# Optimization experiments

Measured on AMD Instinct MI355X. Metric: run time of the kernel, lower is better.

The kernel has to match this reference:

```python
import jax, jax.numpy as jnp
import numpy as np

B, S, D = 2, 2048, 1024
N, M, HD = 16, 4, 64          # query heads, kv heads, head dim
G = N // M                    # GQA group size
V = 32000
GIN = 12                      # gate input dim
ROPE_THETA = 1024.0
ROT = int(HD * 0.5)           # partial rotary dim = 32
EPS = 1e-6
STD = 0.006


def setup_inputs() -> dict:
    key = jax.random.key(0)
    ks = jax.random.split(key, 10)
    tn = lambda k, shape: (STD * jax.random.truncated_normal(k, -3, 3, shape)).astype(jnp.float32)
    return {
        "x": jax.random.normal(ks[0], (B, S, D), jnp.float32),
        "token_ids": jax.random.randint(ks[1], (B, S), 0, V),
        "mask": jnp.tril(jnp.ones((S, S), dtype=bool)),  # causal
        "w_q": tn(ks[2], (D, N * HD)),
        "w_k": tn(ks[3], (D, M * HD)),
        "w_v": tn(ks[4], (D, M * HD)),
        "w_o": tn(ks[5], (N * HD, D)),  # zeros at init; random for a meaningful baseline
        "ve_embed": tn(ks[6], (V, M * HD)),
        "value_lambda": jnp.full((), 0.5, jnp.float32),
        "ve_lambda": jnp.full((), 0.5, jnp.float32),
        "ve_gate": tn(ks[7], (GIN, M)),
        "attn_gate": tn(ks[8], (GIN, N)),
    }


def _qk_norm(t):
    var = jnp.mean(jnp.square(t.astype(jnp.float32)), axis=-1, keepdims=True)
    return (t * jax.lax.rsqrt(var + EPS)).astype(t.dtype)


def _rope(t):
    # partial rotary: rotate first ROT dims only
    half = ROT // 2
    inv_freq = 1.0 / ROPE_THETA ** (jnp.arange(half, dtype=jnp.float32) / half)
    ang = jnp.arange(S, dtype=jnp.float32)[:, None] * inv_freq[None, :]
    cos = jnp.cos(ang)[None, :, None, :]  # [1,S,1,half]
    sin = jnp.sin(ang)[None, :, None, :]
    rot, pas = t[..., :ROT], t[..., ROT:]
    x1, x2 = jnp.split(rot, 2, axis=-1)
    return jnp.concatenate([x1 * cos - x2 * sin, x2 * cos + x1 * sin, pas], axis=-1)


def reference(x, token_ids, mask, w_q, w_k, w_v, w_o, ve_embed,
              value_lambda, ve_lambda, ve_gate, attn_gate):
    q = (x @ w_q).reshape(B, S, N, HD)
    k = (x @ w_k).reshape(B, S, M, HD)
    v = (x @ w_v).reshape(B, S, M, HD)
    q = _rope(_qk_norm(q))
    k = _rope(_qk_norm(k))

    # value-embedding lambda mixing with sigmoid gate
    ve = ve_embed[token_ids].reshape(B, S, M, HD)
    ve_g = 2.0 * jax.nn.sigmoid(x[..., :GIN] @ ve_gate)       # [B,S,M]
    v = value_lambda * v + ve_lambda * ve_g[..., None] * ve

    # GQA causal attention (group q heads over kv heads, no kv repeat)
    qg = q.reshape(B, S, M, G, HD)
    scale = 1.0 / np.sqrt(HD).astype(np.float32)
    scores = jnp.einsum('bqmgd,bkmd->bmgqk', qg, k) * scale   # [B,M,G,S,S]
    scores = jnp.where(mask[None, None, None], scores, jnp.float32(-1e30))
    p = jax.nn.softmax(scores, axis=-1)
    attn = jnp.einsum('bmgqk,bkmd->bqmgd', p, v).reshape(B, S, N, HD)

    # output sigmoid gate then out-projection
    a_g = 2.0 * jax.nn.sigmoid(x[..., :GIN] @ attn_gate)      # [B,S,N]
    attn = a_g[..., None] * attn
    return attn.reshape(B, S, N * HD) @ w_o
```

## Files before the change

### kernel.cpp

```cpp
#include <hip/hip_runtime.h>
#include <math.h>

#define S_LEN 2048
#define NHEADS 16
#define KVH 4

typedef __attribute__((ext_vector_type(8))) _Float16 half8;
typedef __attribute__((ext_vector_type(4))) _Float16 half4;
typedef __attribute__((ext_vector_type(2))) __fp16 fp16x2;
typedef __attribute__((ext_vector_type(4))) float f32x4;

__device__ inline void gld16(const void* g, void* l) {
  __builtin_amdgcn_global_load_lds(
      (const __attribute__((address_space(1))) unsigned int*)g,
      (__attribute__((address_space(3))) unsigned int*)l, 16, 0, 0);
}

__global__ __launch_bounds__(256) void setup_fused(
    const float* __restrict__ wq, const float* __restrict__ wk,
    const float* __restrict__ wv, const float* __restrict__ wo,
    const float* __restrict__ x, const float* __restrict__ attn_gate,
    _Float16* __restrict__ wqkvT, _Float16* __restrict__ woT,
    float2* __restrict__ costab, float* __restrict__ ag,
    _Float16* __restrict__ xh)
{
  const int t = threadIdx.x;
  int L = blockIdx.x;

  if (L >= 1024) {
    const size_t i = ((size_t)(L - 1024) * 256 + t) * 16;
    #pragma unroll
    for (int c = 0; c < 2; c++) {
      float4 f0 = *(const float4*)(x + i + c * 8);
      float4 f1 = *(const float4*)(x + i + c * 8 + 4);
      half8 h;
      h[0] = (_Float16)f0.x; h[1] = (_Float16)f0.y; h[2] = (_Float16)f0.z; h[3] = (_Float16)f0.w;
      h[4] = (_Float16)f1.x; h[5] = (_Float16)f1.y; h[6] = (_Float16)f1.z; h[7] = (_Float16)f1.w;
      *(half8*)(xh + i + c * 8) = h;
    }
    return;
  }
  if (L >= 768) {
    const int row = (L - 768) * 16 + (t >> 4);
    const int n = t & 15;
    float z = 0.f;
    #pragma unroll
    for (int i = 0; i < 12; ++i) z += x[(size_t)row * 1024 + i] * attn_gate[i * NHEADS + n];
    ag[(size_t)row * NHEADS + n] = 2.f / (1.f + __expf(-z));
    return;
  }
  if (L >= 640) {
    const int gi = (L - 640) * 256 + t;
    const int s = gi >> 4, i = gi & 15;
    const float ang = (float)s * exp2f(-0.625f * (float)i);
    float c, sn;
    sincosf(ang, &sn, &c);
    costab[gi] = make_float2(c, sn);
    return;
  }

  const float* in; _Float16* out; int C, ct, rt;
  if (L < 256)      { in = wq; out = wqkvT;                       C = 1024; ct = (L & 15) * 64; rt = (L >> 4) * 64; }
  else if (L < 320) { L -= 256; in = wk; out = wqkvT + (size_t)1024 * 1024; C = 256; ct = (L & 3) * 64; rt = (L >> 2) * 64; }
  else if (L < 384) { L -= 320; in = wv; out = wqkvT + (size_t)1280 * 1024; C = 256; ct = (L & 3) * 64; rt = (L >> 2) * 64; }
  else              { L -= 384; in = wo; out = woT;               C = 1024; ct = (L & 15) * 64; rt = (L >> 4) * 64; }

  __shared__ float Ls[64][65];
  {
    const int r = t >> 2, cs = (t & 3) << 4;
    const float* src = in + (size_t)(rt + r) * C + ct + cs;
    #pragma unroll
    for (int j = 0; j < 16; j += 4) {
      float4 v = *(const float4*)(src + j);
      Ls[r][cs + j] = v.x; Ls[r][cs + j + 1] = v.y;
      Ls[r][cs + j + 2] = v.z; Ls[r][cs + j + 3] = v.w;
    }
  }
  __syncthreads();
  {
    const int c = t >> 2, rs = (t & 3) << 4;
    half8 h0, h1;
    #pragma unroll
    for (int j = 0; j < 8; j++) h0[j] = (_Float16)Ls[rs + j][c];
    #pragma unroll
    for (int j = 0; j < 8; j++) h1[j] = (_Float16)Ls[rs + 8 + j][c];
    _Float16* dst = out + (size_t)(ct + c) * 1024 + rt + rs;
    *(half8*)dst = h0;
    *(half8*)(dst + 8) = h1;
  }
}

template<typename OUT_T, bool EPI>
__global__ __launch_bounds__(256) void gemm_k(
    const _Float16* __restrict__ A, const _Float16* __restrict__ BT,
    OUT_T* __restrict__ C, int M, int N, int K, int lda,
    const float2* __restrict__ costab)
{
  __shared__ _Float16 lds[24576];
  const int t = threadIdx.x;
  const int w = t >> 6, l = t & 63;
  const int lg = l >> 4, ll = l & 15;
  const int bm = blockIdx.y * 64, bn = blockIdx.x * 128;
  const int wr = (w >> 1) * 32, wc = (w & 1) * 64;
  const int srow = l >> 3, sslot = l & 7;

  f32x4 acc[2][4] = {};

  auto stage = [&](int k0, int buf) {
    char* Ab = (char*)lds + buf * 8192;
    char* Bb = (char*)lds + 16384 + buf * 16384;
    #pragma unroll
    for (int i = 0; i < 2; i++) {
      const int row = w * 16 + i * 8 + srow;
      gld16(A + (size_t)(bm + row) * lda + k0 + ((sslot ^ (row & 7)) << 3),
            Ab + w * 2048 + i * 1024);
    }
    #pragma unroll
    for (int i = 0; i < 4; i++) {
      const int row = w * 32 + i * 8 + srow;
      gld16(BT + (size_t)(bn + row) * K + k0 + ((sslot ^ (row & 7)) << 3),
            Bb + w * 4096 + i * 1024);
    }
  };

  stage(0, 0);
  __syncthreads();

  int buf = 0;
  for (int k0 = 0; k0 < K; k0 += 64) {
    if (k0 + 64 < K) stage(k0 + 64, buf ^ 1);

    const char* Ab = (const char*)lds + buf * 8192;
    const char* Bb = (const char*)lds + 16384 + buf * 16384;
    half8 af[2][2], bfr[2][4];
    #pragma unroll
    for (int mt = 0; mt < 2; mt++) {
      const int row = wr + mt * 16 + ll;
      #pragma unroll
      for (int s = 0; s < 2; s++)
        af[mt][s] = *(const half8*)(Ab + row * 128 + (((4 * s + lg) ^ (row & 7)) << 4));
    }
    #pragma unroll
    for (int nt = 0; nt < 4; nt++) {
      const int row = wc + nt * 16 + ll;
      #pragma unroll
      for (int s = 0; s < 2; s++)
        bfr[s][nt] = *(const half8*)(Bb + row * 128 + (((4 * s + lg) ^ (row & 7)) << 4));
    }
    __builtin_amdgcn_s_setprio(1);
    #pragma unroll
    for (int s = 0; s < 2; s++)
      #pragma unroll
      for (int mt = 0; mt < 2; mt++)
        #pragma unroll
        for (int nt = 0; nt < 4; nt++)
          acc[mt][nt] = __builtin_amdgcn_mfma_f32_16x16x32_f16(af[mt][s], bfr[s][nt], acc[mt][nt], 0, 0, 0);
    __builtin_amdgcn_s_setprio(0);

    __syncthreads();
    buf ^= 1;
  }

  if constexpr (EPI) {
    const int col0 = bn + wc;
    const int head = col0 >> 6;
    const bool isv = head >= 20;
    const float qs = (head < 16) ? 0.18033688f : 1.0f;
    #pragma unroll
    for (int mt = 0; mt < 2; mt++) {
      if (isv) {
        #pragma unroll
        for (int r = 0; r < 4; r++) {
          const size_t row = (size_t)bm + wr + mt * 16 + lg * 4 + r;
          #pragma unroll
          for (int nt = 0; nt < 4; nt++)
            C[row * N + col0 + nt * 16 + ll] = (OUT_T)acc[mt][nt][r];
        }
      } else {
        float ss[4];
        #pragma unroll
        for (int r = 0; r < 4; r++)
          ss[r] = acc[mt][0][r] * acc[mt][0][r] + acc[mt][1][r] * acc[mt][1][r]
                + acc[mt][2][r] * acc[mt][2][r] + acc[mt][3][r] * acc[mt][3][r];
        #pragma unroll
        for (int mi = 0; mi < 4; mi++) {
          const int msk = 1 << mi;
          #pragma unroll
          for (int r = 0; r < 4; r++) ss[r] += __shfl_xor(ss[r], msk);
        }
        #pragma unroll
        for (int r = 0; r < 4; r++) {
          const size_t row = (size_t)bm + wr + mt * 16 + lg * 4 + r;
          const float inv = rsqrtf(ss[r] * (1.0f / 64.0f) + 1e-6f) * qs;
          const float2 cs2 = costab[(row & (S_LEN - 1)) * 16 + ll];
          const float a0 = acc[mt][0][r] * inv, a1 = acc[mt][1][r] * inv;
          C[row * N + col0 +      ll] = (OUT_T)(a0 * cs2.x - a1 * cs2.y);
          C[row * N + col0 + 16 + ll] = (OUT_T)(a1 * cs2.x + a0 * cs2.y);
          C[row * N + col0 + 32 + ll] = (OUT_T)(acc[mt][2][r] * inv);
          C[row * N + col0 + 48 + ll] = (OUT_T)(acc[mt][3][r] * inv);
        }
      }
    }
  } else {
    #pragma unroll
    for (int mt = 0; mt < 2; mt++) {
      #pragma unroll
      for (int r = 0; r < 4; r++) {
        const size_t row = (size_t)bm + wr + mt * 16 + lg * 4 + r;
        #pragma unroll
        for (int nt = 0; nt < 4; nt++) {
          const int col = bn + wc + nt * 16 + ll;
          if constexpr (sizeof(OUT_T) == 2) C[row * N + col] = (OUT_T)(_Float16)acc[mt][nt][r];
          else                              C[row * N + col] = acc[mt][nt][r];
        }
      }
    }
  }
}

__global__ __launch_bounds__(256) void vtrans_mix(
    const _Float16* __restrict__ qkv, const float* __restrict__ x,
    const int* __restrict__ token_ids, const float* __restrict__ ve_embed,
    const float* __restrict__ ve_gate, const float* __restrict__ vlam,
    const float* __restrict__ velam, _Float16* __restrict__ vT)
{
  __shared__ _Float16 Ls[64][72];
  __shared__ float veg[64];
  __shared__ int toks[64];
  const int st = blockIdx.x * 64;
  const int bm = blockIdx.y;
  const int b = bm >> 2, m = bm & 3;
  const int t = threadIdx.x;

  if (t < 64) {
    const size_t row_g = (size_t)b * S_LEN + st + t;
    toks[t] = token_ids[row_g];
    float z = 0.f;
    #pragma unroll
    for (int i = 0; i < 12; ++i) z += x[row_g * 1024 + i] * ve_gate[i * KVH + m];
    veg[t] = velam[0] * 2.f / (1.f + __expf(-z));
  }
  __syncthreads();
  {
    const int sr = t >> 2, ds = (t & 3) << 4;
    const float vl = vlam[0];
    const _Float16* src = qkv + ((size_t)(b * S_LEN + st + sr)) * 1536 + 1280 + m * 64 + ds;
    const float* ves = ve_embed + (size_t)toks[sr] * 256 + m * 64 + ds;
    half8 v0 = *(const half8*)src;
    half8 v1 = *(const half8*)(src + 8);
    const float g = veg[sr];
    #pragma unroll
    for (int q4 = 0; q4 < 4; q4++) {
      float4 ev = *(const float4*)(ves + q4 * 4);
      const int o0 = q4 * 4;
      Ls[sr][ds + o0 + 0] = (_Float16)(vl * (float)((o0 + 0 < 8) ? v0[o0 + 0] : v1[o0 - 8]) + g * ev.x);
      Ls[sr][ds + o0 + 1] = (_Float16)(vl * (float)((o0 + 1 < 8) ? v0[o0 + 1] : v1[o0 - 7]) + g * ev.y);
      Ls[sr][ds + o0 + 2] = (_Float16)(vl * (float)((o0 + 2 < 8) ? v0[o0 + 2] : v1[o0 - 6]) + g * ev.z);
      Ls[sr][ds + o0 + 3] = (_Float16)(vl * (float)((o0 + 3 < 8) ? v0[o0 + 3] : v1[o0 - 5]) + g * ev.w);
    }
  }
  __syncthreads();
  {
    const int dr = t >> 2, ssl = (t & 3) << 4;
    half8 o0, o1;
    #pragma unroll
    for (int j = 0; j < 8; j++) { o0[j] = Ls[ssl + j][dr]; o1[j] = Ls[ssl + 8 + j][dr]; }
    _Float16* dst = vT + ((size_t)bm * 64 + dr) * S_LEN + st + ssl;
    *(half8*)dst = o0;
    *(half8*)(dst + 8) = o1;
  }
}

__global__ __launch_bounds__(256) void attn_mfma(
    _Float16* __restrict__ qkv, const _Float16* __restrict__ vT,
    const float* __restrict__ ag)
{
  const int L = blockIdx.x;
  const int qt = 31 - (L >> 5);
  const int b = (L >> 4) & 1;
  const int n = L & 15;
  const int m = n >> 2;

  const int t = threadIdx.x, w = t >> 6, l = t & 63;
  const int lg = l >> 4, ll = l & 15;
  const int g  = w & 1;
  const int kh = w >> 1;

  __shared__ _Float16 lds[20480];

  const int qbl = qt * 64 + g * 32;
  const size_t qrow_g = (size_t)(b * S_LEN) + qbl;

  half8 qa[2][2];
  #pragma unroll
  for (int qf = 0; qf < 2; qf++)
    #pragma unroll
    for (int s = 0; s < 2; s++)
      qa[qf][s] = *(const half8*)(qkv + (qrow_g + qf * 16 + ll) * 1536 + n * 64 + s * 32 + lg * 8);

  float agr[2][4];
  if (kh == 0) {
    #pragma unroll
    for (int qf = 0; qf < 2; qf++)
      #pragma unroll
      for (int r = 0; r < 4; r++)
        agr[qf][r] = ag[(qrow_g + qf * 16 + lg * 4 + r) * NHEADS + n];
  }

  half8 ones;
  #pragma unroll
  for (int i = 0; i < 8; i++) ones[i] = (_Float16)1.0f;

  f32x4 o[2][4] = {};
  f32x4 ol[2] = {};

  const int srow = l >> 3, sslot = l & 7;

  auto stage = [&](int kt, int buf) {
    #pragma unroll
    for (int i = 0; i < 2; i++) {
      const int kr = w * 16 + i * 8 + srow;
      const size_t kg = ((size_t)(b * S_LEN + kt * 64 + kr)) * 1536 + 1024 + m * 64
                        + ((sslot ^ (kr & 7)) << 3);
      gld16(qkv + kg, (char*)lds + buf * 8192 + w * 2048 + i * 1024);
      const int vr = w * 16 + i * 8 + srow;
      const size_t vg = ((size_t)((b * KVH + m) * 64 + vr)) * S_LEN + kt * 64
                        + ((sslot ^ (vr & 7)) << 3);
      gld16(vT + vg, (char*)lds + 16384 + buf * 8192 + w * 2048 + i * 1024);
    }
  };

  stage(0, 0);
  __syncthreads();

  for (int kt = 0; kt <= qt; kt++) {
    const int cur = kt & 1;
    if (kt < qt) stage(kt + 1, cur ^ 1);

    const char* Ksb = (const char*)lds + cur * 8192;
    const char* Vsb = (const char*)lds + 16384 + cur * 8192;
    char* Psb = (char*)lds + 32768;

    f32x4 sc[2][2];
    #pragma unroll
    for (int qf = 0; qf < 2; qf++)
      #pragma unroll
      for (int kf = 0; kf < 2; kf++) {
        sc[qf][kf][0] = -11.6f; sc[qf][kf][1] = -11.6f;
        sc[qf][kf][2] = -11.6f; sc[qf][kf][3] = -11.6f;
      }
    __builtin_amdgcn_s_setprio(1);
    #pragma unroll
    for (int s = 0; s < 2; s++)
      #pragma unroll
      for (int kf = 0; kf < 2; kf++) {
        const int krow = kh * 32 + kf * 16 + ll;
        const half8 kb = *(const half8*)(Ksb + krow * 128
                          + (((4 * s + lg) ^ (krow & 7)) << 4));
        sc[0][kf] = __builtin_amdgcn_mfma_f32_16x16x32_f16(kb, qa[0][s], sc[0][kf], 0, 0, 0);
        sc[1][kf] = __builtin_amdgcn_mfma_f32_16x16x32_f16(kb, qa[1][s], sc[1][kf], 0, 0, 0);
      }
    __builtin_amdgcn_s_setprio(0);

    if (kt == qt) {
      #pragma unroll
      for (int qf = 0; qf < 2; qf++) {
        const int qg = qbl + qf * 16 + ll;
        #pragma unroll
        for (int kf = 0; kf < 2; kf++)
          #pragma unroll
          for (int r = 0; r < 4; r++)
            if (kt * 64 + kh * 32 + kf * 16 + 4 * lg + r > qg) sc[qf][kf][r] = -1e30f;
      }
    }

    #pragma unroll
    for (int qf = 0; qf < 2; qf++) {
      const int q_loc = g * 32 + qf * 16 + ll;
      #pragma unroll
      for (int kf = 0; kf < 2; kf++) {
        union { fp16x2 h2[2]; half4 h4; } P;
        P.h2[0] = __builtin_amdgcn_cvt_pkrtz(exp2f(sc[qf][kf][0]), exp2f(sc[qf][kf][1]));
        P.h2[1] = __builtin_amdgcn_cvt_pkrtz(exp2f(sc[qf][kf][2]), exp2f(sc[qf][kf][3]));
        const int slot = (4 * kh + 2 * kf + (lg >> 1)) ^ (q_loc & 7);
        *(half4*)(Psb + q_loc * 128 + slot * 16 + (lg & 1) * 8) = P.h4;
      }
    }

    __builtin_amdgcn_s_setprio(1);
    {
      half8 pa[2];
      #pragma unroll
      for (int qf = 0; qf < 2; qf++) {
        const int prow = g * 32 + qf * 16 + ll;
        pa[qf] = *(const half8*)(Psb + prow * 128 + (((4 * kh + lg) ^ (prow & 7)) << 4));
      }
      ol[0] = __builtin_amdgcn_mfma_f32_16x16x32_f16(pa[0], ones, ol[0], 0, 0, 0);
      ol[1] = __builtin_amdgcn_mfma_f32_16x16x32_f16(pa[1], ones, ol[1], 0, 0, 0);
      #pragma unroll
      for (int df = 0; df < 4; df++) {
        const int vrow = df * 16 + ll;
        const half8 vb = *(const half8*)(Vsb + vrow * 128
                          + (((4 * kh + lg) ^ (vrow & 7)) << 4));
        o[0][df] = __builtin_amdgcn_mfma_f32_16x16x32_f16(pa[0], vb, o[0][df], 0, 0, 0);
        o[1][df] = __builtin_amdgcn_mfma_f32_16x16x32_f16(pa[1], vb, o[1][df], 0, 0, 0);
      }
    }
    __builtin_amdgcn_s_setprio(0);

    __syncthreads();
  }

  char* red = (char*)lds;
  if (kh == 1) {
    #pragma unroll
    for (int qf = 0; qf < 2; qf++) {
      #pragma unroll
      for (int df = 0; df < 4; df++)
        #pragma unroll
        for (int r = 0; r < 4; r++)
          *(float*)(red + g * 8192 + (qf * 16 + lg * 4 + r) * 256 + (df * 16 + ll) * 4)
              = o[qf][df][r];
      if (ll == 0)
        #pragma unroll
        for (int r = 0; r < 4; r++)
          *(float*)(red + 16384 + g * 128 + (qf * 16 + lg * 4 + r) * 4) = ol[qf][r];
    }
  }
  __syncthreads();
  if (kh == 0) {
    #pragma unroll
    for (int qf = 0; qf < 2; qf++)
      #pragma unroll
      for (int r = 0; r < 4; r++) {
        const int qloc32 = qf * 16 + lg * 4 + r;
        const float lsum = ol[qf][r] + *(const float*)(red + 16384 + g * 128 + qloc32 * 4);
        const size_t qrow = qrow_g + qf * 16 + lg * 4 + r;
        const float scale = agr[qf][r] / lsum;
        #pragma unroll
        for (int df = 0; df < 4; df++) {
          const float ov = o[qf][df][r]
              + *(const float*)(red + g * 8192 + qloc32 * 256 + (df * 16 + ll) * 4);
          qkv[qrow * 1536 + n * 64 + df * 16 + ll] = (_Float16)(ov * scale);
        }
      }
  }
}

extern "C" void kernel_launch(void* const* d_in, const int* in_sizes, int n_in,
                              void* d_out, int out_size, void* d_ws, size_t ws_size,
                              hipStream_t stream) {
  const float* x         = (const float*)d_in[0];
  const int*   token_ids = (const int*)d_in[1];
  const float* w_q       = (const float*)d_in[3];
  const float* w_k       = (const float*)d_in[4];
  const float* w_v       = (const float*)d_in[5];
  const float* w_o       = (const float*)d_in[6];
  const float* ve_embed  = (const float*)d_in[7];
  const float* vlam      = (const float*)d_in[8];
  const float* velam     = (const float*)d_in[9];
  const float* ve_gate   = (const float*)d_in[10];
  const float* attn_gate = (const float*)d_in[11];
  float* out = (float*)d_out;

  char* p = (char*)d_ws;
  _Float16* wqkvT = (_Float16*)p; p += (size_t)1536 * 1024 * 2;
  _Float16* woT   = (_Float16*)p; p += (size_t)1024 * 1024 * 2;
  _Float16* qkv   = (_Float16*)p; p += (size_t)4096 * 1536 * 2;
  _Float16* vTb   = (_Float16*)p; p += (size_t)8 * 64 * S_LEN * 2;
  float*    ag    = (float*)p;    p += (size_t)4096 * NHEADS * 4;

  _Float16* xh = (_Float16*)d_out;
  float2* costab = (float2*)((char*)d_out + (size_t)12 * 1024 * 1024);

  dim3 blk(256);
  setup_fused<<<dim3(2048), blk, 0, stream>>>(w_q, w_k, w_v, w_o, x, attn_gate,
                                              wqkvT, woT, costab, ag, xh);

  gemm_k<_Float16, true><<<dim3(12, 64), blk, 0, stream>>>(
      xh, wqkvT, qkv, 4096, 1536, 1024, 1024, costab);

  vtrans_mix<<<dim3(32, 8), blk, 0, stream>>>(qkv, x, token_ids, ve_embed,
                                              ve_gate, vlam, velam, vTb);

  attn_mfma<<<dim3(1024), blk, 0, stream>>>(qkv, vTb, ag);

  gemm_k<float, false><<<dim3(8, 64), blk, 0, stream>>>(
      qkv, woT, out, 4096, 1024, 1024, 1536, nullptr);
}
```

Baseline: 92.96 us.

## Fuse value-embedding mix and V transpose into QKV GEMM epilogue

Removes the separate vtrans_mix kernel. The value-embedding gate is now computed in the setup kernel alongside the attention gate and stored in a small buffer. The QKV GEMM epilogue for V columns gathers ve_embed rows, applies the lambda mix, and writes transposed fp16 V directly as half4 stores. This saves a kernel launch and a round trip of V through global memory, but the GEMM epilogue now does scattered 4-byte ve_embed gathers and strided transposed stores, which may be poorly coalesced.

```diff
diff --git a/kernel.cpp b/kernel.cpp
--- a/kernel.cpp
+++ b/kernel.cpp
@@ -20,9 +20,10 @@
     const float* __restrict__ wq, const float* __restrict__ wk,
     const float* __restrict__ wv, const float* __restrict__ wo,
     const float* __restrict__ x, const float* __restrict__ attn_gate,
+    const float* __restrict__ ve_gate, const float* __restrict__ velam,
     _Float16* __restrict__ wqkvT, _Float16* __restrict__ woT,
     float2* __restrict__ costab, float* __restrict__ ag,
-    _Float16* __restrict__ xh)
+    float* __restrict__ veg4, _Float16* __restrict__ xh)
 {
   const int t = threadIdx.x;
   int L = blockIdx.x;
@@ -47,6 +48,12 @@
     #pragma unroll
     for (int i = 0; i < 12; ++i) z += x[(size_t)row * 1024 + i] * attn_gate[i * NHEADS + n];
     ag[(size_t)row * NHEADS + n] = 2.f / (1.f + __expf(-z));
+    if (n < KVH) {
+      float z2 = 0.f;
+      #pragma unroll
+      for (int i = 0; i < 12; ++i) z2 += x[(size_t)row * 1024 + i] * ve_gate[i * KVH + n];
+      veg4[(size_t)row * KVH + n] = velam[0] * 2.f / (1.f + __expf(-z2));
+    }
     return;
   }
   if (L >= 640) {
@@ -94,7 +101,9 @@
 __global__ __launch_bounds__(256) void gemm_k(
     const _Float16* __restrict__ A, const _Float16* __restrict__ BT,
     OUT_T* __restrict__ C, int M, int N, int K, int lda,
-    const float2* __restrict__ costab)
+    const float2* __restrict__ costab, const int* __restrict__ token_ids,
+    const float* __restrict__ ve_embed, const float* __restrict__ veg4,
+    const float* __restrict__ vlam, _Float16* __restrict__ vT)
 {
   __shared__ _Float16 lds[24576];
   const int t = threadIdx.x;
@@ -164,19 +173,39 @@
   if constexpr (EPI) {
     const int col0 = bn + wc;
     const int head = col0 >> 6;
-    const bool isv = head >= 20;
-    const float qs = (head < 16) ? 0.18033688f : 1.0f;
-    #pragma unroll
-    for (int mt = 0; mt < 2; mt++) {
-      if (isv) {
+    if (head >= 20) {
+      const int mloc = head - 20;
+      const int bq = bm >> 11;
+      const int vbm = bq * KVH + mloc;
+      const int sl0 = bm - bq * S_LEN;
+      const float vl = vlam[0];
+      #pragma unroll
+      for (int mt = 0; mt < 2; mt++) {
+        const int s_base = sl0 + wr + mt * 16 + lg * 4;
+        int   tok[4];
+        float vg[4];
         #pragma unroll
         for (int r = 0; r < 4; r++) {
-          const size_t row = (size_t)bm + wr + mt * 16 + lg * 4 + r;
+          const size_t grow = (size_t)bq * S_LEN + s_base + r;
+          tok[r] = token_ids[grow];
+          vg[r]  = veg4[grow * KVH + mloc];
+        }
+        #pragma unroll
+        for (int nt = 0; nt < 4; nt++) {
+          const int d = nt * 16 + ll;
+          half4 o4;
           #pragma unroll
-          for (int nt = 0; nt < 4; nt++)
-            C[row * N + col0 + nt * 16 + ll] = (OUT_T)acc[mt][nt][r];
-        }
-      } else {
+          for (int r = 0; r < 4; r++) {
+            const float e = ve_embed[(size_t)tok[r] * 256 + mloc * 64 + d];
+            o4[r] = (_Float16)(vl * acc[mt][nt][r] + vg[r] * e);
+          }
+          *(half4*)(vT + ((size_t)vbm * 64 + d) * S_LEN + s_base) = o4;
+        }
+      }
+    } else {
+      const float qs = (head < 16) ? 0.18033688f : 1.0f;
+      #pragma unroll
+      for (int mt = 0; mt < 2; mt++) {
         float ss[4];
         #pragma unroll
         for (int r = 0; r < 4; r++)
@@ -215,59 +244,6 @@
         }
       }
     }
-  }
-}
-
-__global__ __launch_bounds__(256) void vtrans_mix(
-    const _Float16* __restrict__ qkv, const float* __restrict__ x,
-    const int* __restrict__ token_ids, const float* __restrict__ ve_embed,
-    const float* __restrict__ ve_gate, const float* __restrict__ vlam,
-    const float* __restrict__ velam, _Float16* __restrict__ vT)
-{
-  __shared__ _Float16 Ls[64][72];
-  __shared__ float veg[64];
-  __shared__ int toks[64];
-  const int st = blockIdx.x * 64;
-  const int bm = blockIdx.y;
-  const int b = bm >> 2, m = bm & 3;
-  const int t = threadIdx.x;
-
-  if (t < 64) {
-    const size_t row_g = (size_t)b * S_LEN + st + t;
-    toks[t] = token_ids[row_g];
-    float z = 0.f;
-    #pragma unroll
-    for (int i = 0; i < 12; ++i) z += x[row_g * 1024 + i] * ve_gate[i * KVH + m];
-    veg[t] = velam[0] * 2.f / (1.f + __expf(-z));
-  }
-  __syncthreads();
-  {
-    const int sr = t >> 2, ds = (t & 3) << 4;
-    const float vl = vlam[0];
-    const _Float16* src = qkv + ((size_t)(b * S_LEN + st + sr)) * 1536 + 1280 + m * 64 + ds;
-    const float* ves = ve_embed + (size_t)toks[sr] * 256 + m * 64 + ds;
-    half8 v0 = *(const half8*)src;
-    half8 v1 = *(const half8*)(src + 8);
-    const float g = veg[sr];
-    #pragma unroll
-    for (int q4 = 0; q4 < 4; q4++) {
-      float4 ev = *(const float4*)(ves + q4 * 4);
-      const int o0 = q4 * 4;
-      Ls[sr][ds + o0 + 0] = (_Float16)(vl * (float)((o0 + 0 < 8) ? v0[o0 + 0] : v1[o0 - 8]) + g * ev.x);
-      Ls[sr][ds + o0 + 1] = (_Float16)(vl * (float)((o0 + 1 < 8) ? v0[o0 + 1] : v1[o0 - 7]) + g * ev.y);
-      Ls[sr][ds + o0 + 2] = (_Float16)(vl * (float)((o0 + 2 < 8) ? v0[o0 + 2] : v1[o0 - 6]) + g * ev.z);
-      Ls[sr][ds + o0 + 3] = (_Float16)(vl * (float)((o0 + 3 < 8) ? v0[o0 + 3] : v1[o0 - 5]) + g * ev.w);
-    }
-  }
-  __syncthreads();
-  {
-    const int dr = t >> 2, ssl = (t & 3) << 4;
-    half8 o0, o1;
-    #pragma unroll
-    for (int j = 0; j < 8; j++) { o0[j] = Ls[ssl + j][dr]; o1[j] = Ls[ssl + 8 + j][dr]; }
-    _Float16* dst = vT + ((size_t)bm * 64 + dr) * S_LEN + st + ssl;
-    *(half8*)dst = o0;
-    *(half8*)(dst + 8) = o1;
   }
 }
 
@@ -469,22 +445,23 @@
   _Float16* qkv   = (_Float16*)p; p += (size_t)4096 * 1536 * 2;
   _Float16* vTb   = (_Float16*)p; p += (size_t)8 * 64 * S_LEN * 2;
   float*    ag    = (float*)p;    p += (size_t)4096 * NHEADS * 4;
+  float*    veg4  = (float*)p;    p += (size_t)4096 * KVH * 4;
 
   _Float16* xh = (_Float16*)d_out;
   float2* costab = (float2*)((char*)d_out + (size_t)12 * 1024 * 1024);
 
   dim3 blk(256);
   setup_fused<<<dim3(2048), blk, 0, stream>>>(w_q, w_k, w_v, w_o, x, attn_gate,
-                                              wqkvT, woT, costab, ag, xh);
+                                              ve_gate, velam,
+                                              wqkvT, woT, costab, ag, veg4, xh);
 
   gemm_k<_Float16, true><<<dim3(12, 64), blk, 0, stream>>>(
-      xh, wqkvT, qkv, 4096, 1536, 1024, 1024, costab);
-
-  vtrans_mix<<<dim3(32, 8), blk, 0, stream>>>(qkv, x, token_ids, ve_embed,
-                                              ve_gate, vlam, velam, vTb);
+      xh, wqkvT, qkv, 4096, 1536, 1024, 1024,
+      costab, token_ids, ve_embed, veg4, vlam, vTb);
 
   attn_mfma<<<dim3(1024), blk, 0, stream>>>(qkv, vTb, ag);
 
   gemm_k<float, false><<<dim3(8, 64), blk, 0, stream>>>(
-      qkv, woT, out, 4096, 1024, 1024, 1536, nullptr);
+      qkv, woT, out, 4096, 1024, 1024, 1536,
+      nullptr, nullptr, nullptr, nullptr, nullptr, nullptr);
 }
```

Measured after the change: 89.40 us, median of 2. -3.8%, faster.
